# Kernel tuning notes

Measured on AMD Instinct MI355X. Metric: run time of the kernel, lower is better.

Reference implementation:

```python
import jax, jax.numpy as jnp
import numpy as np
from jax.ops import segment_sum

N_NODES = 100000
N_EDGES = 3200000
DIM = 256
N_CLASSES = 32
N_GRAPHS = 64


def setup_inputs() -> dict:
    key = jax.random.key(0)
    k1, k2, k3, k4, k5 = jax.random.split(key, 5)
    x = jax.random.normal(k1, (N_NODES, DIM), dtype=jnp.float32)
    W = jax.random.normal(k2, (DIM, N_CLASSES), dtype=jnp.float32) / np.sqrt(DIM)
    b = jax.random.normal(k3, (N_CLASSES,), dtype=jnp.float32) * 0.01
    edge_index = jax.random.randint(k4, (2, N_EDGES), 0, N_NODES, dtype=jnp.int64)
    batch = jnp.sort(jax.random.randint(k5, (N_NODES,), 0, N_GRAPHS, dtype=jnp.int64))
    return {"x": x, "W": W, "b": b, "edge_index": edge_index, "batch": batch}


def reference(x, W, b, edge_index, batch):
    N = x.shape[0]
    # GCNConv: linear transform (no bias), then normalized aggregation, then bias
    h = x @ W  # [N, C]
    # add self loops (PyG default add_self_loops=True)
    loop = jnp.arange(N, dtype=edge_index.dtype)
    src = jnp.concatenate([edge_index[0], loop])  # source (message sender)
    dst = jnp.concatenate([edge_index[1], loop])  # target (aggregation site)
    # symmetric normalization: deg computed at target with unit edge weights
    deg = segment_sum(jnp.ones_like(dst, dtype=h.dtype), dst, num_segments=N)
    dinv = jnp.where(deg > 0, jax.lax.rsqrt(deg), 0.0)
    norm = dinv[src] * dinv[dst]  # [E+N]
    msg = h[src] * norm[:, None]  # gather + scale
    out = segment_sum(msg, dst, num_segments=N) + b  # scatter-add, bias after agg
    # global_mean_pool: segment mean over graphs
    cnt = segment_sum(jnp.ones((N,), dtype=out.dtype), batch, num_segments=N_GRAPHS)
    sums = segment_sum(out, batch, num_segments=N_GRAPHS)
    return sums / jnp.maximum(cnt, 1.0)[:, None]
```

## Files before the change

kernel.cpp:

```cpp
#include <hip/hip_runtime.h>

#define NN    100000
#define NE    3200000
#define DIMK  256
#define NC    32
#define NG    64

#define ROWS   64
#define NBUCK  1563
#define CAP    2432
#define NB1    512
#define EPB    6250
#define NSL    16
#define MAXG   768
#define NCH    8

static constexpr size_t OFF_REC    = 0;
static constexpr size_t OFF_DINV   = 15204864;
static constexpr size_t OFF_BTOT   = 15604864;
static constexpr size_t OFF_START  = 15613056;
static constexpr size_t OFF_CTRL   = 15613568;
static constexpr size_t OFF_P2     = 15613696;
static constexpr size_t OFF_PART   = 16662272;
static constexpr size_t OFF_DEGARR = OFF_PART;
static constexpr size_t OFF_CNT    = OFF_PART + 400000;
static constexpr size_t OFF_EXC    = OFF_PART + 3601024;

__device__ __forceinline__ int idx_at(const void* p, long i, bool i64) {
    return i64 ? (int)((const long long*)p)[i] : ((const int*)p)[i];
}

__device__ __forceinline__ bool detect_i64(const void* ei) {
    const int* w = (const int*)ei;
    return (w[1] == 0) & (w[3] == 0) & (w[5] == 0) &
           (w[7] == 0) & (w[9] == 0) & (w[11] == 0);
}

__global__ __launch_bounds__(256) void k_pre(const void* __restrict__ ei,
        unsigned int* __restrict__ parts, int* __restrict__ cnt) {
    __shared__ unsigned int h[12500];
    const bool i64 = detect_i64(ei);
    const int b = blockIdx.x;
    if (b < 256) {
        const int hh = b >> 7;
        const int sl = b & 127;
        const int lo = hh * 50000, hi = lo + 50000;
        for (int t = threadIdx.x; t < 12500; t += 256) h[t] = 0u;
        __syncthreads();
        const int e0 = sl * 25000;
        for (int e = e0 + threadIdx.x; e < e0 + 25000; e += 256) {
            int d = idx_at(ei, (long)NE + e, i64);
            if (d >= lo && d < hi) {
                int r = d - lo;
                atomicAdd(&h[r >> 2], 1u << ((r & 3) * 8));
            }
        }
        __syncthreads();
        for (int t = threadIdx.x; t < 12500; t += 256)
            parts[(size_t)b * 12500 + t] = h[t];
    } else {
        const int k = b - 256;
        for (int t = threadIdx.x; t < NBUCK; t += 256) h[t] = 0u;
        __syncthreads();
        const int e0 = k * EPB;
        for (int e = e0 + threadIdx.x; e < e0 + EPB; e += 256) {
            int s = idx_at(ei, e, i64);
            atomicAdd(&h[s >> 6], 1u);
        }
        __syncthreads();
        for (int t = threadIdx.x; t < NBUCK; t += 256)
            cnt[t * NB1 + k] = (int)h[t];
    }
}

__global__ __launch_bounds__(512) void k_mid(const unsigned int* __restrict__ parts,
        unsigned int* __restrict__ degarr, float* __restrict__ dinv,
        const void* __restrict__ batch, const void* __restrict__ ei,
        int* __restrict__ start, const int* __restrict__ cnt,
        int* __restrict__ exc, int* __restrict__ btot) {
    __shared__ int s[512];
    const int b = blockIdx.x;
    const int t = threadIdx.x;
    if (b < 49) {
        int i = b * 512 + t;
        if (i >= 25000) return;
        int h = (i >= 12500) ? 1 : 0;
        int w = i - h * 12500;
        int c0 = 0, c1 = 0, c2 = 0, c3 = 0;
        const unsigned int* base = parts + (size_t)(h * 128) * 12500 + w;
#pragma unroll 4
        for (int q = 0; q < 128; ++q) {
            unsigned int v = base[(size_t)q * 12500];
            c0 += v & 255u; c1 += (v >> 8) & 255u; c2 += (v >> 16) & 255u; c3 += v >> 24;
        }
        int node = h * 50000 + w * 4;
        degarr[node]     = 1u + c0;  dinv[node]     = 1.0f / sqrtf((float)(1 + c0));
        degarr[node + 1] = 1u + c1;  dinv[node + 1] = 1.0f / sqrtf((float)(1 + c1));
        degarr[node + 2] = 1u + c2;  dinv[node + 2] = 1.0f / sqrtf((float)(1 + c2));
        degarr[node + 3] = 1u + c3;  dinv[node + 3] = 1.0f / sqrtf((float)(1 + c3));
    } else if (b < 245) {
        const bool i64 = detect_i64(ei);
        int i = (b - 49) * 512 + t;
        if (i >= NN) return;
        int bi = idx_at(batch, i, i64);
        int bp = (i == 0) ? -1 : idx_at(batch, i - 1, i64);
        for (int g = bp + 1; g <= bi; ++g) start[g] = i;
        if (i == NN - 1)
            for (int g = bi + 1; g <= NG; ++g) start[g] = NN;
    } else {
        const int bkt = b - 245;
        int v = cnt[bkt * NB1 + t];
        s[t] = v;
        __syncthreads();
        for (int off = 1; off < 512; off <<= 1) {
            int u = (t >= off) ? s[t - off] : 0;
            __syncthreads();
            s[t] += u;
            __syncthreads();
        }
        exc[bkt * NB1 + t] = bkt * CAP + (s[t] - v);
        if (t == 511) btot[bkt] = s[511];
    }
}

__global__ __launch_bounds__(256) void k_place(const void* __restrict__ ei,
        const void* __restrict__ batch, const unsigned int* __restrict__ degarr,
        const int* __restrict__ exc, unsigned int* __restrict__ rec,
        int* __restrict__ ctrl) {
    __shared__ unsigned int lc[NBUCK];
    __shared__ int lbase[NBUCK];
    const bool i64 = detect_i64(ei);
    const int k = blockIdx.x;
    if (k == 0 && threadIdx.x == 0) ctrl[1] = 0;
    for (int t = threadIdx.x; t < NBUCK; t += 256) {
        lc[t] = 0u;
        lbase[t] = exc[t * NB1 + k];
    }
    __syncthreads();
    const int e0 = k * EPB;
    for (int e = e0 + threadIdx.x; e < e0 + EPB; e += 256) {
        int s = idx_at(ei, e, i64);
        int d = idx_at(ei, (long)NE + e, i64);
        int g = idx_at(batch, d, i64);
        unsigned int deg = min(degarr[d], 1048575u);
        int b = s >> 6;
        unsigned int r = atomicAdd(&lc[b], 1u);
        rec[lbase[b] + (int)r] = (deg << 12) | (unsigned)((s & 63) * 64 + g);
    }
}

__global__ __launch_bounds__(512, 4) void k_fused(
        const float* __restrict__ x, const float* __restrict__ dinv,
        const void* __restrict__ batch, const void* __restrict__ ei,
        const unsigned int* __restrict__ rec, const int* __restrict__ btot,
        float* __restrict__ part, int* __restrict__ ctrl) {
    __shared__ __align__(16) float Ach[ROWS * 64];
    __shared__ __align__(16) float4 xs4[2 * 512];
    const bool i64 = detect_i64(ei);
    const int tid = threadIdx.x;
    const int gi = tid >> 6;
    const int di = tid & 63;
    const int myrow = tid >> 6;
    const int mycol = tid & 63;

    float acc[8][4];
#pragma unroll
    for (int g = 0; g < 8; ++g)
#pragma unroll
        for (int k = 0; k < 4; ++k) acc[g][k] = 0.0f;

    const float4* x4 = (const float4*)x;
    float4* Ach4 = (float4*)Ach;
    const float4 z4 = make_float4(0.f, 0.f, 0.f, 0.f);

    for (;;) {
        if (tid == 0) *(int*)xs4 = atomicAdd(&ctrl[1], 1);
        __syncthreads();
        const int bkt = *(const int*)xs4;
        if (bkt >= NBUCK) break;
        const int j0 = bkt * ROWS;

        Ach4[tid] = z4;
        Ach4[tid + 512] = z4;
        __syncthreads();
        if (tid < ROWS) {
            int j = j0 + tid;
            if (j < NN) Ach[tid * 64 + idx_at(batch, j, i64)] = dinv[j];
        }
        __syncthreads();
        {
            const int rb = bkt * CAP;
            const int re = rb + btot[bkt];
            for (int r = rb + tid; r < re; r += 512) {
                unsigned int q = rec[r];
                float val = 1.0f / sqrtf((float)(q >> 12));
                atomicAdd(&Ach[q & 4095u], val);
            }
        }
        __syncthreads();
#pragma unroll
        for (int k = 0; k < 8; ++k) {
            int e = tid + (k << 9);
            int j = j0 + (e >> 6);
            float dv = (j < NN) ? dinv[j] : 0.0f;
            Ach[e] *= dv;
        }
        {
            int jA = min(j0 + myrow, NN - 1);
            xs4[tid] = x4[(size_t)jA * 64 + mycol];
        }
        __syncthreads();

        for (int c = 0; c < NCH; ++c) {
            int cn = min(c + 1, NCH - 1);
            int jA = min(j0 + cn * 8 + myrow, NN - 1);
            float4 pf = x4[(size_t)jA * 64 + mycol];
            const float4* xr = xs4 + ((c & 1) << 9);
#pragma unroll
            for (int jj = 0; jj < 8; ++jj) {
                const float* arow = Ach + ((c << 3) + jj) * 64 + (gi << 3);
                float4 p0 = *(const float4*)arow;
                float4 p1 = *(const float4*)(arow + 4);
                float4 xv = xr[jj * 64 + di];
                float pg[8] = {p0.x, p0.y, p0.z, p0.w, p1.x, p1.y, p1.z, p1.w};
#pragma unroll
                for (int g = 0; g < 8; ++g) {
                    acc[g][0] = fmaf(pg[g], xv.x, acc[g][0]);
                    acc[g][1] = fmaf(pg[g], xv.y, acc[g][1]);
                    acc[g][2] = fmaf(pg[g], xv.z, acc[g][2]);
                    acc[g][3] = fmaf(pg[g], xv.w, acc[g][3]);
                }
            }
            xs4[(((c + 1) & 1) << 9) + tid] = pf;
            __syncthreads();
        }
    }

    float* p = part + (size_t)blockIdx.x * (NG * DIMK);
#pragma unroll
    for (int g = 0; g < 8; ++g) {
        float4 w = make_float4(acc[g][0], acc[g][1], acc[g][2], acc[g][3]);
        ((float4*)(p + (gi * 8 + g) * DIMK))[di] = w;
    }
}

__global__ __launch_bounds__(256) void k_reduce1(const float4* __restrict__ part,
        float4* __restrict__ p2, int nblk) {
    int id = blockIdx.x * 256 + threadIdx.x;
    int c4 = id & 4095;
    int sl = id >> 12;
    int span = (nblk + NSL - 1) / NSL;
    int b0 = sl * span, b1 = min(b0 + span, nblk);
    float4 s = make_float4(0.f, 0.f, 0.f, 0.f);
    for (int b = b0; b < b1; ++b) {
        float4 v = part[(size_t)b * 4096 + c4];
        s.x += v.x; s.y += v.y; s.z += v.z; s.w += v.w;
    }
    p2[(size_t)sl * 4096 + c4] = s;
}

__global__ __launch_bounds__(256) void k_final(const float* __restrict__ p2,
        const float* __restrict__ W, const float* __restrict__ bias,
        const int* __restrict__ start, float* __restrict__ out) {
    __shared__ float Sb[8 * DIMK];
    const int tid = threadIdx.x, b = blockIdx.x;
    for (int t = tid; t < 8 * DIMK; t += 256) {
        int gl = t >> 8, d = t & 255;
        float s = 0.f;
#pragma unroll
        for (int sl = 0; sl < NSL; ++sl)
            s += p2[(size_t)sl * (NG * DIMK) + (b * 8 + gl) * DIMK + d];
        Sb[t] = s;
    }
    __syncthreads();
    int g = tid >> 5, c = tid & 31;
    float sum = 0.f;
#pragma unroll 8
    for (int d = 0; d < DIMK; ++d)
        sum = fmaf(Sb[g * DIMK + d], W[d * NC + c], sum);
    int gg = b * 8 + g;
    float cn = (float)max(start[gg + 1] - start[gg], 1);
    out[gg * NC + c] = sum / cn + bias[c];
}

extern "C" void kernel_launch(void* const* d_in, const int* in_sizes, int n_in,
                              void* d_out, int out_size, void* d_ws, size_t ws_size,
                              hipStream_t stream) {
    const float* x    = (const float*)d_in[0];
    const float* W    = (const float*)d_in[1];
    const float* bias = (const float*)d_in[2];
    const void*  ei   = d_in[3];
    const void*  batch= d_in[4];
    float* out = (float*)d_out;

    char* ws = (char*)d_ws;
    unsigned int* rec  = (unsigned int*)(ws + OFF_REC);
    unsigned int* degp = (unsigned int*)(ws + OFF_REC);
    float* dinv  = (float*)(ws + OFF_DINV);
    int*   btot  = (int*)(ws + OFF_BTOT);
    int*   start = (int*)(ws + OFF_START);
    int*   ctrl  = (int*)(ws + OFF_CTRL);
    float* p2    = (float*)(ws + OFF_P2);
    float* part  = (float*)(ws + OFF_PART);
    unsigned int* degarr = (unsigned int*)(ws + OFF_DEGARR);
    int*   cnt   = (int*)(ws + OFF_CNT);
    int*   exc   = (int*)(ws + OFF_EXC);

    long avail = (long)(ws_size - OFF_PART) / 65536;
    int grid = (int)avail;
    if (grid > MAXG) grid = MAXG;
    if (grid < 64) grid = 64;

    k_pre    <<<768, 256, 0, stream>>>(ei, degp, cnt);
    k_mid    <<<1808, 512, 0, stream>>>(degp, degarr, dinv, batch, ei, start,
                                        cnt, exc, btot);
    k_place  <<<NB1, 256, 0, stream>>>(ei, batch, degarr, exc, rec, ctrl);
    k_fused  <<<grid, 512, 0, stream>>>(x, dinv, batch, ei, rec, btot, part, ctrl);
    k_reduce1<<<256, 256, 0, stream>>>((const float4*)part, (float4*)p2, grid);
    k_final  <<<8, 256, 0, stream>>>(p2, W, bias, start, out);
}
```

Measured before the change: 218.8 us.

## Read x rows directly from global with 8-wide per-thread tiles, dropping LDS staging

```diff
diff --git a/kernel.cpp b/kernel.cpp
--- a/kernel.cpp
+++ b/kernel.cpp
@@ -13,7 +13,6 @@
 #define EPB    6250
 #define NSL    16
 #define MAXG   768
-#define NCH    8
 
 static constexpr size_t OFF_REC    = 0;
 static constexpr size_t OFF_DINV   = 15204864;
@@ -155,28 +154,28 @@
         const unsigned int* __restrict__ rec, const int* __restrict__ btot,
         float* __restrict__ part, int* __restrict__ ctrl) {
     __shared__ __align__(16) float Ach[ROWS * 64];
-    __shared__ __align__(16) float4 xs4[2 * 512];
+    __shared__ int sbkt;
     const bool i64 = detect_i64(ei);
-    const int tid = threadIdx.x;
-    const int gi = tid >> 6;
-    const int di = tid & 63;
-    const int myrow = tid >> 6;
-    const int mycol = tid & 63;
-
-    float acc[8][4];
+    const int tid  = threadIdx.x;
+    const int gi   = tid >> 6;
+    const int lane = tid & 63;
+    const int rh   = lane >> 5;
+    const int di   = lane & 31;
+
+    float acc[8][8];
 #pragma unroll
     for (int g = 0; g < 8; ++g)
 #pragma unroll
-        for (int k = 0; k < 4; ++k) acc[g][k] = 0.0f;
+        for (int d = 0; d < 8; ++d) acc[g][d] = 0.0f;
 
     const float4* x4 = (const float4*)x;
     float4* Ach4 = (float4*)Ach;
     const float4 z4 = make_float4(0.f, 0.f, 0.f, 0.f);
 
     for (;;) {
-        if (tid == 0) *(int*)xs4 = atomicAdd(&ctrl[1], 1);
-        __syncthreads();
-        const int bkt = *(const int*)xs4;
+        if (tid == 0) sbkt = atomicAdd(&ctrl[1], 1);
+        __syncthreads();
+        const int bkt = sbkt;
         if (bkt >= NBUCK) break;
         const int j0 = bkt * ROWS;
 
@@ -205,42 +204,43 @@
             float dv = (j < NN) ? dinv[j] : 0.0f;
             Ach[e] *= dv;
         }
-        {
-            int jA = min(j0 + myrow, NN - 1);
-            xs4[tid] = x4[(size_t)jA * 64 + mycol];
-        }
-        __syncthreads();
-
-        for (int c = 0; c < NCH; ++c) {
-            int cn = min(c + 1, NCH - 1);
-            int jA = min(j0 + cn * 8 + myrow, NN - 1);
-            float4 pf = x4[(size_t)jA * 64 + mycol];
-            const float4* xr = xs4 + ((c & 1) << 9);
-#pragma unroll
-            for (int jj = 0; jj < 8; ++jj) {
-                const float* arow = Ach + ((c << 3) + jj) * 64 + (gi << 3);
-                float4 p0 = *(const float4*)arow;
-                float4 p1 = *(const float4*)(arow + 4);
-                float4 xv = xr[jj * 64 + di];
-                float pg[8] = {p0.x, p0.y, p0.z, p0.w, p1.x, p1.y, p1.z, p1.w};
-#pragma unroll
-                for (int g = 0; g < 8; ++g) {
-                    acc[g][0] = fmaf(pg[g], xv.x, acc[g][0]);
-                    acc[g][1] = fmaf(pg[g], xv.y, acc[g][1]);
-                    acc[g][2] = fmaf(pg[g], xv.z, acc[g][2]);
-                    acc[g][3] = fmaf(pg[g], xv.w, acc[g][3]);
-                }
-            }
-            xs4[(((c + 1) & 1) << 9) + tid] = pf;
-            __syncthreads();
-        }
-    }
+        __syncthreads();
+
+        const int jb = j0 + rh * 32;
+#pragma unroll 2
+        for (int jj = 0; jj < 32; ++jj) {
+            int j = min(jb + jj, NN - 1);
+            float4 xa = x4[(size_t)j * 64 + di * 2];
+            float4 xb = x4[(size_t)j * 64 + di * 2 + 1];
+            const float* arow = Ach + (rh * 32 + jj) * 64 + gi * 8;
+            float4 p0 = *(const float4*)arow;
+            float4 p1 = *(const float4*)(arow + 4);
+            float pg[8] = {p0.x, p0.y, p0.z, p0.w, p1.x, p1.y, p1.z, p1.w};
+            float xv[8] = {xa.x, xa.y, xa.z, xa.w, xb.x, xb.y, xb.z, xb.w};
+#pragma unroll
+            for (int g = 0; g < 8; ++g)
+#pragma unroll
+                for (int d = 0; d < 8; ++d)
+                    acc[g][d] = fmaf(pg[g], xv[d], acc[g][d]);
+        }
+        __syncthreads();
+    }
+
+#pragma unroll
+    for (int g = 0; g < 8; ++g)
+#pragma unroll
+        for (int d = 0; d < 8; ++d)
+            acc[g][d] += __shfl_xor(acc[g][d], 32, 64);
 
     float* p = part + (size_t)blockIdx.x * (NG * DIMK);
 #pragma unroll
-    for (int g = 0; g < 8; ++g) {
-        float4 w = make_float4(acc[g][0], acc[g][1], acc[g][2], acc[g][3]);
-        ((float4*)(p + (gi * 8 + g) * DIMK))[di] = w;
+    for (int g = 0; g < 4; ++g) {
+        int gg = rh * 4 + g;
+        float4 w0 = make_float4(acc[gg][0], acc[gg][1], acc[gg][2], acc[gg][3]);
+        float4 w1 = make_float4(acc[gg][4], acc[gg][5], acc[gg][6], acc[gg][7]);
+        float* row = p + (gi * 8 + gg) * DIMK + di * 8;
+        *(float4*)row = w0;
+        *(float4*)(row + 4) = w1;
     }
 }
 
```

New measurement: 363.2 us. +66.0%, slower.
